# Kernel tuning notes

Measured on AMD Instinct MI355X. Metric: run time of the kernel, lower is better.

Reference implementation:

```python
import jax, jax.numpy as jnp
import numpy as np

B, S, HID = 2, 2048, 1024
NH = 16
HD = HID // NH  # 64
ROPE_BASE = 10000.0
NEG_INF = -1e9


def _rope_emb(seq_len):
    # emb = cat(sin, cos) over head_dim, shape [1, S, 1, HD]
    inv_freq = 1.0 / (ROPE_BASE ** (jnp.arange(0, HD, 2, dtype=jnp.float32) / HD))
    pos = jnp.arange(seq_len, dtype=jnp.float32)
    sincos = pos[:, None] * inv_freq[None, :]            # [S, HD/2]
    emb = jnp.concatenate([jnp.sin(sincos), jnp.cos(sincos)], axis=-1)  # [S, HD]
    return emb[None, :, None, :]


def _apply_rope(x, emb):
    # Faithful to the (quirky) torch code: cos = emb[..., 1::2], sin = emb[..., ::2]
    cos = emb[..., 1::2]
    sin = emb[..., ::2]
    xe = x[..., ::2]
    xo = x[..., 1::2]
    return jnp.concatenate([xe * cos - xo * sin, xe * sin + xo * cos], axis=-1)


def setup_inputs() -> dict:
    key = jax.random.key(0)
    ks = jax.random.split(key, 5)
    hidden_states = jax.random.normal(ks[0], (B, S, HID), dtype=jnp.float32)
    # causal additive mask, broadcast over batch/heads
    causal = jnp.tril(jnp.ones((S, S), dtype=bool))
    attention_mask = jnp.where(causal, 0.0, NEG_INF).astype(jnp.float32)[None, None]
    scale = 1.0 / np.sqrt(HID)
    w_q = jax.random.normal(ks[1], (HID, HID), dtype=jnp.float32) * scale
    w_k = jax.random.normal(ks[2], (HID, HID), dtype=jnp.float32) * scale
    w_v = jax.random.normal(ks[3], (HID, HID), dtype=jnp.float32) * scale
    w_o = jax.random.normal(ks[4], (HID, HID), dtype=jnp.float32) * scale
    return {"hidden_states": hidden_states, "attention_mask": attention_mask,
            "w_q": w_q, "w_k": w_k, "w_v": w_v, "w_o": w_o}


def reference(hidden_states, attention_mask, w_q, w_k, w_v, w_o):
    b, s, _ = hidden_states.shape
    # torch Linear: x @ W.T (W is [out, in])
    q = (hidden_states @ w_q.T).reshape(b, s, NH, HD)
    k = (hidden_states @ w_k.T).reshape(b, s, NH, HD)
    v = (hidden_states @ w_v.T).reshape(b, s, NH, HD)
    emb = _rope_emb(s)
    q = _apply_rope(q, emb)
    k = _apply_rope(k, emb)
    # [b, h, s, d]
    q = q.transpose(0, 2, 1, 3)
    k = k.transpose(0, 2, 1, 3)
    v = v.transpose(0, 2, 1, 3)
    scores = jnp.einsum('bhqd,bhkd->bhqk', q, k) / np.sqrt(HD)
    scores = scores + attention_mask
    attn = jax.nn.softmax(scores, axis=-1)
    out = jnp.einsum('bhqk,bhkd->bhqd', attn, v)
    out = out.transpose(0, 2, 1, 3).reshape(b, s, HID)
    return out @ w_o.T
```

## Files before the change

### kernel.cpp

```cpp
#include <hip/hip_runtime.h>
#include <hip/hip_bf16.h>
#include <math.h>

typedef unsigned short u16;
typedef unsigned int   u32;
typedef unsigned long long u64;
typedef __attribute__((ext_vector_type(8))) short bf16x8;
typedef __attribute__((ext_vector_type(4))) short bf16x4;
typedef __attribute__((ext_vector_type(4))) float f32x4;

#define B_   2
#define S_   2048
#define HID_ 1024
#define NH_  16
#define HD_  64
#define MR_  (B_*S_)

#define QSCALE 0.1803368801111137f
#define MBIAS 32.0f

__device__ __forceinline__ u16 f2bf(float f) {
  union { float f; u32 u; } x; x.f = f;
  u32 r = x.u + 0x7fffu + ((x.u >> 16) & 1u);
  return (u16)(r >> 16);
}
__device__ __forceinline__ void gload16(const void* g, void* l) {
  __builtin_amdgcn_global_load_lds(
      (const __attribute__((address_space(1))) u32*)g,
      (__attribute__((address_space(3))) u32*)l, 16, 0, 0);
}

__global__ void k_cvt_all(const float* __restrict__ hs, const float* __restrict__ wq,
                          const float* __restrict__ wk, const float* __restrict__ wv,
                          const float* __restrict__ wo, ushort4* __restrict__ dst) {
  int i = blockIdx.x * blockDim.x + threadIdx.x;
  const float4* src;
  int idx;
  if (i < 1048576) {
    src = (const float4*)hs; idx = i;
  } else {
    int j = i - 1048576;
    int w = j >> 18; idx = j & 262143;
    src = (const float4*)(w == 0 ? wq : w == 1 ? wk : w == 2 ? wv : wo);
  }
  float4 v = src[idx];
  ushort4 o;
  o.x = f2bf(v.x); o.y = f2bf(v.y); o.z = f2bf(v.z); o.w = f2bf(v.w);
  dst[i] = o;
}

__global__ void k_rope_table(float2* __restrict__ tab) {
  int t = blockIdx.x * blockDim.x + threadIdx.x;
  int p = t >> 5, j = t & 31;
  double fp = (double)p;
  double c, s;
  if (j < 16) {
    s = sin(fp * pow(10000.0, -(2.0 * j) / 32.0));
    c = sin(fp * pow(10000.0, -(2.0 * j + 1.0) / 32.0));
  } else {
    s = cos(fp * pow(10000.0, -(2.0 * j - 32.0) / 32.0));
    c = cos(fp * pow(10000.0, -(2.0 * j - 31.0) / 32.0));
  }
  tab[p * 32 + j] = make_float2((float)c, (float)s);
}

template <int MODE, int BM>
__global__ __launch_bounds__(512) void k_gemm_bt(
    const u16* __restrict__ A,
    const u16* __restrict__ W0, const u16* __restrict__ W1, const u16* __restrict__ W2,
    u16* __restrict__ O0, u16* __restrict__ O1, u16* __restrict__ O2,
    float* __restrict__ OF, const float2* __restrict__ tab, int K) {
  constexpr int WR = BM / 4;
  constexpr int MI = BM / 64;
  __shared__ __align__(16) u16 Al[2][BM * 64];
  __shared__ __align__(16) u16 Bl[2][128 * 64];

  int tid = threadIdx.x;
  int lane = tid & 63, wave = tid >> 6;
  int m0 = blockIdx.y * BM;
  int nt0 = blockIdx.x * 128;
  int wi = nt0 >> 10;
  const u16* W = (wi == 0) ? W0 : (wi == 1 ? W1 : W2);
  int n0 = nt0 & 1023;
  int wm = wave >> 1, wn = wave & 1;
  int lg = lane >> 4, lr = lane & 15;

  f32x4 acc[MI][4];
  const f32x4 vz = {0.f, 0.f, 0.f, 0.f};
#pragma unroll
  for (int i = 0; i < MI; ++i)
#pragma unroll
    for (int j = 0; j < 4; ++j) acc[i][j] = vz;

  auto STAGE = [&](int t_, int bs_) {
    int k0 = t_ * 64;
#pragma unroll
    for (int it = 0; it < BM / 64; ++it) {
      int c = it * 512 + tid;
      int row = c >> 3;
      int cw = (c & 7) ^ (row & 7);
      gload16(&A[(size_t)(m0 + row) * K + k0 + cw * 8], &Al[bs_][(it * 512 + wave * 64) * 8]);
    }
#pragma unroll
    for (int it = 0; it < 2; ++it) {
      int c = it * 512 + tid;
      int row = c >> 3;
      int cw = (c & 7) ^ (row & 7);
      gload16(&W[(size_t)(n0 + row) * K + k0 + cw * 8], &Bl[bs_][(it * 512 + wave * 64) * 8]);
    }
  };

  int nkt = K >> 6;
  STAGE(0, 0);

  for (int t = 0; t < nkt; ++t) {
    int cur = t & 1;
    asm volatile("s_waitcnt vmcnt(0)" ::: "memory");
    __builtin_amdgcn_s_barrier();
    __builtin_amdgcn_sched_barrier(0);
    if (t + 1 < nkt) STAGE(t + 1, cur ^ 1);

#pragma unroll
    for (int kk = 0; kk < 2; ++kk) {
      bf16x8 af[MI], bfr[4];
#pragma unroll
      for (int mi = 0; mi < MI; ++mi) {
        int row = wm * WR + mi * 16 + lr;
        int ci = (kk * 4 + lg) ^ (row & 7);
        af[mi] = *(const bf16x8*)&Al[cur][row * 64 + ci * 8];
      }
#pragma unroll
      for (int ni = 0; ni < 4; ++ni) {
        int row = wn * 64 + ni * 16 + lr;
        int ci = (kk * 4 + lg) ^ (row & 7);
        bfr[ni] = *(const bf16x8*)&Bl[cur][row * 64 + ci * 8];
      }
      __builtin_amdgcn_s_setprio(1);
#pragma unroll
      for (int mi = 0; mi < MI; ++mi)
#pragma unroll
        for (int ni = 0; ni < 4; ++ni)
          acc[mi][ni] = __builtin_amdgcn_mfma_f32_16x16x32_bf16(af[mi], bfr[ni], acc[mi][ni], 0, 0, 0);
      __builtin_amdgcn_s_setprio(0);
    }
  }

  if (MODE == 1) {
#pragma unroll
    for (int mi = 0; mi < MI; ++mi)
#pragma unroll
      for (int ni = 0; ni < 4; ++ni)
#pragma unroll
        for (int r = 0; r < 4; ++r) {
          int grow = m0 + wm * WR + mi * 16 + lg * 4 + r;
          int gcol = n0 + wn * 64 + ni * 16 + lr;
          OF[(size_t)grow * 1024 + gcol] = acc[mi][ni][r];
        }
    return;
  }

  if (wi == 2) {
#pragma unroll
    for (int mi = 0; mi < MI; ++mi) {
      int grow0 = m0 + wm * WR + mi * 16 + lg * 4;
      int bb = grow0 >> 11;
      int s = grow0 & 2047;
#pragma unroll
      for (int ni = 0; ni < 4; ++ni) {
        int gcol = n0 + wn * 64 + ni * 16 + lr;
        int h = gcol >> 6, dd = gcol & 63;
        u64 pk = (u64)f2bf(acc[mi][ni][0]) |
                 ((u64)f2bf(acc[mi][ni][1]) << 16) |
                 ((u64)f2bf(acc[mi][ni][2]) << 32) |
                 ((u64)f2bf(acc[mi][ni][3]) << 48);
        *(u64*)&O2[((size_t)(bb * NH_ + h) * HD_ + dd) * S_ + s] = pk;
      }
    }
  } else {
    u16* OB = wi ? O1 : O0;
    float sc = wi ? 1.0f : QSCALE;
#pragma unroll
    for (int mi = 0; mi < MI; ++mi) {
#pragma unroll
      for (int ni = 0; ni < 4; ++ni) {
        int gcol = n0 + wn * 64 + ni * 16 + lr;
        int h = gcol >> 6;
        int j = (gcol & 63) >> 1;
        bool even = !(gcol & 1);
        int ocol = h * 64 + (even ? j : 32 + j);
#pragma unroll
        for (int r = 0; r < 4; ++r) {
          float val = acc[mi][ni][r];
          float pv = __shfl_xor(val, 1);
          int grow = m0 + wm * WR + mi * 16 + lg * 4 + r;
          int s = grow & 2047;
          float2 cs = tab[s * 32 + j];
          float xe = even ? val : pv;
          float xo = even ? pv : val;
          float res = even ? (xe * cs.x - xo * cs.y) : (xe * cs.y + xo * cs.x);
          OB[(size_t)grow * 1024 + ocol] = f2bf(res * sc);
        }
      }
    }
  }
}

__global__ __launch_bounds__(256, 4) void k_attn(
    const u16* __restrict__ Q, const u16* __restrict__ Kr, const u16* __restrict__ VT,
    u16* __restrict__ O) {
  __shared__ __align__(16) u16 Kl[2][64 * 64];
  __shared__ __align__(16) u16 Vl[2][64 * 64];

  int tid = threadIdx.x, lane = tid & 63, wave = tid >> 6;
  int id = blockIdx.x;
  int qt = 31 - (id >> 5);
  int bh = id & 31;
  int b = bh >> 4, h = bh & 15;
  int lg = lane >> 4, lr = lane & 15;
  int bS = b * S_;
  int nkt = qt + 1;
  int q0 = qt * 64 + wave * 16;

  const u16* vtb = &VT[(size_t)bh * HD_ * S_];
  int l8 = lane >> 3, l7 = lane & 7;
  int sl = l7 ^ l8;

  auto STAGE = [&](int kt_, int bs_) {
#pragma unroll
    for (int it = 0; it < 2; ++it) {
      int rb = wave * 16 + it * 8;
      int r = rb + l8;
      gload16(&Kr[(size_t)(bS + kt_ * 64 + r) * HID_ + h * HD_ + sl * 8],
              &Kl[bs_][rb * 64]);
      gload16(&vtb[(size_t)r * S_ + kt_ * 64 + sl * 8],
              &Vl[bs_][rb * 64]);
    }
  };

  STAGE(0, 0);

  bf16x8 qf[2];
#pragma unroll
  for (int kk = 0; kk < 2; ++kk)
    qf[kk] = *(const bf16x8*)
        &Q[(size_t)(bS + q0 + lr) * HID_ + h * HD_ + kk * 32 + lg * 8];

  f32x4 acc[4];
  const f32x4 vz = {0.f, 0.f, 0.f, 0.f};
#pragma unroll
  for (int df = 0; df < 4; ++df) acc[df] = vz;
  float l_ = 0.f;

  for (int kt = 0; kt < nkt; ++kt) {
    int cur = kt & 1;
    if (kt + 1 < nkt) {
      STAGE(kt + 1, cur ^ 1);
      asm volatile("s_waitcnt vmcnt(4)" ::: "memory");
    } else {
      asm volatile("s_waitcnt vmcnt(0)" ::: "memory");
    }
    __builtin_amdgcn_s_barrier();
    __builtin_amdgcn_sched_barrier(0);

    bf16x8 kfr[4][2];
#pragma unroll
    for (int kf = 0; kf < 4; ++kf) {
      int row = kf * 16 + lr;
#pragma unroll
      for (int kk = 0; kk < 2; ++kk) {
        int ci = (kk * 4 + lg) ^ (row & 7);
        kfr[kf][kk] = *(const bf16x8*)&Kl[cur][row * 64 + ci * 8];
      }
    }

    f32x4 st[4];
#pragma unroll
    for (int kf = 0; kf < 4; ++kf) st[kf] = vz;
    __builtin_amdgcn_s_setprio(1);
#pragma unroll
    for (int kk = 0; kk < 2; ++kk)
#pragma unroll
      for (int kf = 0; kf < 4; ++kf)
        st[kf] = __builtin_amdgcn_mfma_f32_16x16x32_bf16(
            kfr[kf][kk], qf[kk], st[kf], 0, 0, 0);
    __builtin_amdgcn_s_setprio(0);

    if (kt == qt) {
      int qg = q0 + lr;
#pragma unroll
      for (int kf = 0; kf < 4; ++kf)
#pragma unroll
        for (int r = 0; r < 4; ++r) {
          int kg = kt * 64 + kf * 16 + lg * 4 + r;
          if (kg > qg) st[kf][r] = -1e30f;
        }
    }

    float ts = 0.f;
    bf16x4 pb[4];
#pragma unroll
    for (int kf = 0; kf < 4; ++kf) {
#pragma unroll
      for (int r = 0; r < 4; ++r) {
        float e = __builtin_amdgcn_exp2f(st[kf][r] - MBIAS);
        st[kf][r] = e;
        ts += e;
      }
      u32 w0, w1;
      asm("v_cvt_pk_bf16_f32 %0, %1, %2" : "=v"(w0) : "v"(st[kf][0]), "v"(st[kf][1]));
      asm("v_cvt_pk_bf16_f32 %0, %1, %2" : "=v"(w1) : "v"(st[kf][2]), "v"(st[kf][3]));
      union { u32 u[2]; bf16x4 v; } pk;
      pk.u[0] = w0; pk.u[1] = w1;
      pb[kf] = pk.v;
    }
    l_ += ts;

    __builtin_amdgcn_s_setprio(1);
#pragma unroll
    for (int df = 0; df < 4; ++df) {
      int row = df * 16 + lr;
#pragma unroll
      for (int kf = 0; kf < 4; ++kf) {
        int slot = (kf * 2 + (lg >> 1)) ^ (row & 7);
        bf16x4 vfr = *(const bf16x4*)&Vl[cur][row * 64 + slot * 8 + (lg & 1) * 4];
        acc[df] = __builtin_amdgcn_mfma_f32_16x16x16bf16_1k(
            vfr, pb[kf], acc[df], 0, 0, 0);
      }
    }
    __builtin_amdgcn_s_setprio(0);

    __builtin_amdgcn_sched_barrier(0);
    __builtin_amdgcn_s_barrier();
  }

  l_ += __shfl_xor(l_, 16);
  l_ += __shfl_xor(l_, 32);
  float inv = 1.0f / l_;
  int grow = bS + q0 + lr;
#pragma unroll
  for (int df = 0; df < 4; ++df) {
    u64 pk = (u64)f2bf(acc[df][0] * inv) |
             ((u64)f2bf(acc[df][1] * inv) << 16) |
             ((u64)f2bf(acc[df][2] * inv) << 32) |
             ((u64)f2bf(acc[df][3] * inv) << 48);
    *(u64*)&O[(size_t)grow * HID_ + h * HD_ + df * 16 + lg * 4] = pk;
  }
}

extern "C" void kernel_launch(void* const* d_in, const int* in_sizes, int n_in,
                              void* d_out, int out_size, void* d_ws, size_t ws_size,
                              hipStream_t stream) {
  const float* hs = (const float*)d_in[0];
  const float* wq = (const float*)d_in[2];
  const float* wk = (const float*)d_in[3];
  const float* wv = (const float*)d_in[4];
  const float* wo = (const float*)d_in[5];
  float* out = (float*)d_out;

  char* ws = (char*)d_ws;
  const size_t P = (size_t)MR_ * HID_ * 2;
  u16* Xb  = (u16*)(ws);
  u16* Wqb = (u16*)(ws + P);
  u16* Wkb = (u16*)(ws + P + (size_t)HID_ * HID_ * 2);
  u16* Wvb = (u16*)(ws + P + (size_t)HID_ * HID_ * 4);
  u16* Wob = (u16*)(ws + P + (size_t)HID_ * HID_ * 6);
  u16* q_r = (u16*)(ws + 2 * P);
  u16* k_r = (u16*)(ws + 3 * P);
  u16* vt  = (u16*)(ws + 4 * P);
  float2* tab = (float2*)(ws + 5 * P);
  u16* attn_o = Xb;

  k_cvt_all<<<8192, 256, 0, stream>>>(hs, wq, wk, wv, wo, (ushort4*)ws);
  k_rope_table<<<256, 256, 0, stream>>>(tab);

  k_gemm_bt<0, 128><<<dim3(24, 32), 512, 0, stream>>>(
      Xb, Wqb, Wkb, Wvb, q_r, k_r, vt, nullptr, tab, HID_);

  k_attn<<<1024, 256, 0, stream>>>(q_r, k_r, vt, attn_o);

  k_gemm_bt<1, 64><<<dim3(8, 64), 512, 0, stream>>>(
      attn_o, Wob, Wob, Wob, nullptr, nullptr, nullptr, out, nullptr, HID_);
}
```

Before: 115.1 us.

## Use 256x256 tiles with split-K half-stage pipelining for QKV projection

Replaces the templated QKV GEMM (128x128 tiles, 768 blocks) with a dedicated kernel using 256x256 output tiles across 192 blocks. Each 64-wide K step is split into two 32-wide halves with interleaved loads and partial vmcnt waits, so global loads overlap MFMA work. Blocks are assigned to tiles in a grouped order meant to improve L2 reuse. The larger tiles cut redundant global and LDS traffic, but 192 blocks may underfill the CUs and raise register pressure; the O projection is split out unchanged into its own kernel.

After: 119.8 us. +4.1%, slower.

```diff
diff --git a/kernel.cpp b/kernel.cpp
--- a/kernel.cpp
+++ b/kernel.cpp
@@ -64,105 +64,146 @@
   tab[p * 32 + j] = make_float2((float)c, (float)s);
 }
 
-template <int MODE, int BM>
-__global__ __launch_bounds__(512) void k_gemm_bt(
+__global__ __launch_bounds__(512) void k_qkv(
     const u16* __restrict__ A,
     const u16* __restrict__ W0, const u16* __restrict__ W1, const u16* __restrict__ W2,
     u16* __restrict__ O0, u16* __restrict__ O1, u16* __restrict__ O2,
-    float* __restrict__ OF, const float2* __restrict__ tab, int K) {
-  constexpr int WR = BM / 4;
-  constexpr int MI = BM / 64;
-  __shared__ __align__(16) u16 Al[2][BM * 64];
-  __shared__ __align__(16) u16 Bl[2][128 * 64];
+    const float2* __restrict__ tab) {
+  __shared__ __align__(16) u16 Alds[2][2][256 * 32];
+  __shared__ __align__(16) u16 Blds[2][2][256 * 32];
 
   int tid = threadIdx.x;
   int lane = tid & 63, wave = tid >> 6;
-  int m0 = blockIdx.y * BM;
-  int nt0 = blockIdx.x * 128;
-  int wi = nt0 >> 10;
+  int id = blockIdx.x;
+  int g = id >> 3, x = id & 7;
+  int mt = 2 * x + (g & 1);
+  int nt = g >> 1;
+  int m0 = mt * 256;
+  int wi = nt >> 2;
   const u16* W = (wi == 0) ? W0 : (wi == 1 ? W1 : W2);
-  int n0 = nt0 & 1023;
-  int wm = wave >> 1, wn = wave & 1;
+  int n0 = (nt & 3) * 256;
+  int wm = wave >> 2, wn = wave & 3;
   int lg = lane >> 4, lr = lane & 15;
 
-  f32x4 acc[MI][4];
+  f32x4 acc[8][4];
   const f32x4 vz = {0.f, 0.f, 0.f, 0.f};
 #pragma unroll
-  for (int i = 0; i < MI; ++i)
+  for (int i = 0; i < 8; ++i)
 #pragma unroll
     for (int j = 0; j < 4; ++j) acc[i][j] = vz;
 
-  auto STAGE = [&](int t_, int bs_) {
-    int k0 = t_ * 64;
-#pragma unroll
-    for (int it = 0; it < BM / 64; ++it) {
-      int c = it * 512 + tid;
-      int row = c >> 3;
-      int cw = (c & 7) ^ (row & 7);
-      gload16(&A[(size_t)(m0 + row) * K + k0 + cw * 8], &Al[bs_][(it * 512 + wave * 64) * 8]);
-    }
+  auto SA = [&](int j_, int d_, int hk_) {
 #pragma unroll
     for (int it = 0; it < 2; ++it) {
       int c = it * 512 + tid;
-      int row = c >> 3;
-      int cw = (c & 7) ^ (row & 7);
-      gload16(&W[(size_t)(n0 + row) * K + k0 + cw * 8], &Bl[bs_][(it * 512 + wave * 64) * 8]);
+      int row = c >> 2, sl = c & 3;
+      int cw = sl ^ ((row >> 1) & 3);
+      gload16(&A[(size_t)(m0 + row) * HID_ + j_ * 64 + hk_ * 32 + cw * 8],
+              &Alds[d_][hk_][(it * 512 + wave * 64) * 8]);
     }
   };
-
-  int nkt = K >> 6;
-  STAGE(0, 0);
-
-  for (int t = 0; t < nkt; ++t) {
-    int cur = t & 1;
-    asm volatile("s_waitcnt vmcnt(0)" ::: "memory");
+  auto SB = [&](int j_, int d_, int hk_) {
+#pragma unroll
+    for (int it = 0; it < 2; ++it) {
+      int c = it * 512 + tid;
+      int row = c >> 2, sl = c & 3;
+      int cw = sl ^ ((row >> 1) & 3);
+      gload16(&W[(size_t)(n0 + row) * HID_ + j_ * 64 + hk_ * 32 + cw * 8],
+              &Blds[d_][hk_][(it * 512 + wave * 64) * 8]);
+    }
+  };
+
+  SA(0, 0, 0); SB(0, 0, 0); SA(0, 0, 1); SB(0, 0, 1);
+
+  for (int j = 0; j < 16; ++j) {
+    int cur = j & 1, nxt = cur ^ 1;
+    bool more = (j < 15);
+    bf16x8 bfr[4], afr[4];
+
+    asm volatile("s_waitcnt vmcnt(4)" ::: "memory");
     __builtin_amdgcn_s_barrier();
     __builtin_amdgcn_sched_barrier(0);
-    if (t + 1 < nkt) STAGE(t + 1, cur ^ 1);
-
-#pragma unroll
-    for (int kk = 0; kk < 2; ++kk) {
-      bf16x8 af[MI], bfr[4];
-#pragma unroll
-      for (int mi = 0; mi < MI; ++mi) {
-        int row = wm * WR + mi * 16 + lr;
-        int ci = (kk * 4 + lg) ^ (row & 7);
-        af[mi] = *(const bf16x8*)&Al[cur][row * 64 + ci * 8];
-      }
-#pragma unroll
-      for (int ni = 0; ni < 4; ++ni) {
-        int row = wn * 64 + ni * 16 + lr;
-        int ci = (kk * 4 + lg) ^ (row & 7);
-        bfr[ni] = *(const bf16x8*)&Bl[cur][row * 64 + ci * 8];
-      }
-      __builtin_amdgcn_s_setprio(1);
-#pragma unroll
-      for (int mi = 0; mi < MI; ++mi)
-#pragma unroll
-        for (int ni = 0; ni < 4; ++ni)
-          acc[mi][ni] = __builtin_amdgcn_mfma_f32_16x16x32_bf16(af[mi], bfr[ni], acc[mi][ni], 0, 0, 0);
-      __builtin_amdgcn_s_setprio(0);
-    }
-  }
-
-  if (MODE == 1) {
-#pragma unroll
-    for (int mi = 0; mi < MI; ++mi)
+    if (more) SA(j + 1, nxt, 0);
+#pragma unroll
+    for (int ni = 0; ni < 4; ++ni) {
+      int row = wn * 64 + ni * 16 + lr;
+      int ci = lg ^ ((row >> 1) & 3);
+      bfr[ni] = *(const bf16x8*)&Blds[cur][0][row * 32 + ci * 8];
+    }
+#pragma unroll
+    for (int mi = 0; mi < 4; ++mi) {
+      int row = wm * 128 + mi * 16 + lr;
+      int ci = lg ^ ((row >> 1) & 3);
+      afr[mi] = *(const bf16x8*)&Alds[cur][0][row * 32 + ci * 8];
+    }
+    __builtin_amdgcn_s_setprio(1);
+#pragma unroll
+    for (int mi = 0; mi < 4; ++mi)
 #pragma unroll
       for (int ni = 0; ni < 4; ++ni)
-#pragma unroll
-        for (int r = 0; r < 4; ++r) {
-          int grow = m0 + wm * WR + mi * 16 + lg * 4 + r;
-          int gcol = n0 + wn * 64 + ni * 16 + lr;
-          OF[(size_t)grow * 1024 + gcol] = acc[mi][ni][r];
-        }
-    return;
+        acc[mi][ni] = __builtin_amdgcn_mfma_f32_16x16x32_bf16(afr[mi], bfr[ni], acc[mi][ni], 0, 0, 0);
+    __builtin_amdgcn_s_setprio(0);
+
+    if (more) SB(j + 1, nxt, 0);
+#pragma unroll
+    for (int mi = 0; mi < 4; ++mi) {
+      int row = wm * 128 + (mi + 4) * 16 + lr;
+      int ci = lg ^ ((row >> 1) & 3);
+      afr[mi] = *(const bf16x8*)&Alds[cur][0][row * 32 + ci * 8];
+    }
+    __builtin_amdgcn_s_setprio(1);
+#pragma unroll
+    for (int mi = 0; mi < 4; ++mi)
+#pragma unroll
+      for (int ni = 0; ni < 4; ++ni)
+        acc[mi + 4][ni] = __builtin_amdgcn_mfma_f32_16x16x32_bf16(afr[mi], bfr[ni], acc[mi + 4][ni], 0, 0, 0);
+    __builtin_amdgcn_s_setprio(0);
+
+    if (more) { asm volatile("s_waitcnt vmcnt(4)" ::: "memory"); }
+    else      { asm volatile("s_waitcnt vmcnt(0)" ::: "memory"); }
+    __builtin_amdgcn_s_barrier();
+    __builtin_amdgcn_sched_barrier(0);
+    if (more) SA(j + 1, nxt, 1);
+#pragma unroll
+    for (int ni = 0; ni < 4; ++ni) {
+      int row = wn * 64 + ni * 16 + lr;
+      int ci = lg ^ ((row >> 1) & 3);
+      bfr[ni] = *(const bf16x8*)&Blds[cur][1][row * 32 + ci * 8];
+    }
+#pragma unroll
+    for (int mi = 0; mi < 4; ++mi) {
+      int row = wm * 128 + mi * 16 + lr;
+      int ci = lg ^ ((row >> 1) & 3);
+      afr[mi] = *(const bf16x8*)&Alds[cur][1][row * 32 + ci * 8];
+    }
+    __builtin_amdgcn_s_setprio(1);
+#pragma unroll
+    for (int mi = 0; mi < 4; ++mi)
+#pragma unroll
+      for (int ni = 0; ni < 4; ++ni)
+        acc[mi][ni] = __builtin_amdgcn_mfma_f32_16x16x32_bf16(afr[mi], bfr[ni], acc[mi][ni], 0, 0, 0);
+    __builtin_amdgcn_s_setprio(0);
+
+    if (more) SB(j + 1, nxt, 1);
+#pragma unroll
+    for (int mi = 0; mi < 4; ++mi) {
+      int row = wm * 128 + (mi + 4) * 16 + lr;
+      int ci = lg ^ ((row >> 1) & 3);
+      afr[mi] = *(const bf16x8*)&Alds[cur][1][row * 32 + ci * 8];
+    }
+    __builtin_amdgcn_s_setprio(1);
+#pragma unroll
+    for (int mi = 0; mi < 4; ++mi)
+#pragma unroll
+      for (int ni = 0; ni < 4; ++ni)
+        acc[mi + 4][ni] = __builtin_amdgcn_mfma_f32_16x16x32_bf16(afr[mi], bfr[ni], acc[mi + 4][ni], 0, 0, 0);
+    __builtin_amdgcn_s_setprio(0);
   }
 
   if (wi == 2) {
 #pragma unroll
-    for (int mi = 0; mi < MI; ++mi) {
-      int grow0 = m0 + wm * WR + mi * 16 + lg * 4;
+    for (int mi = 0; mi < 8; ++mi) {
+      int grow0 = m0 + wm * 128 + mi * 16 + lg * 4;
       int bb = grow0 >> 11;
       int s = grow0 & 2047;
 #pragma unroll
@@ -180,7 +221,7 @@
     u16* OB = wi ? O1 : O0;
     float sc = wi ? 1.0f : QSCALE;
 #pragma unroll
-    for (int mi = 0; mi < MI; ++mi) {
+    for (int mi = 0; mi < 8; ++mi) {
 #pragma unroll
       for (int ni = 0; ni < 4; ++ni) {
         int gcol = n0 + wn * 64 + ni * 16 + lr;
@@ -192,7 +233,7 @@
         for (int r = 0; r < 4; ++r) {
           float val = acc[mi][ni][r];
           float pv = __shfl_xor(val, 1);
-          int grow = m0 + wm * WR + mi * 16 + lg * 4 + r;
+          int grow = m0 + wm * 128 + mi * 16 + lg * 4 + r;
           int s = grow & 2047;
           float2 cs = tab[s * 32 + j];
           float xe = even ? val : pv;
@@ -203,6 +244,83 @@
       }
     }
   }
+}
+
+__global__ __launch_bounds__(512) void k_oproj(
+    const u16* __restrict__ A, const u16* __restrict__ W0,
+    float* __restrict__ OF, int K) {
+  __shared__ __align__(16) u16 Al[2][64 * 64];
+  __shared__ __align__(16) u16 Bl[2][128 * 64];
+
+  int tid = threadIdx.x;
+  int lane = tid & 63, wave = tid >> 6;
+  int m0 = blockIdx.y * 64;
+  int n0 = blockIdx.x * 128;
+  int wm = wave >> 1, wn = wave & 1;
+  int lg = lane >> 4, lr = lane & 15;
+
+  f32x4 acc[4];
+  const f32x4 vz = {0.f, 0.f, 0.f, 0.f};
+#pragma unroll
+  for (int j = 0; j < 4; ++j) acc[j] = vz;
+
+  auto STAGE = [&](int t_, int bs_) {
+    int k0 = t_ * 64;
+    {
+      int c = tid;
+      int row = c >> 3;
+      int cw = (c & 7) ^ (row & 7);
+      gload16(&A[(size_t)(m0 + row) * K + k0 + cw * 8], &Al[bs_][(wave * 64) * 8]);
+    }
+#pragma unroll
+    for (int it = 0; it < 2; ++it) {
+      int c = it * 512 + tid;
+      int row = c >> 3;
+      int cw = (c & 7) ^ (row & 7);
+      gload16(&W0[(size_t)(n0 + row) * K + k0 + cw * 8], &Bl[bs_][(it * 512 + wave * 64) * 8]);
+    }
+  };
+
+  int nkt = K >> 6;
+  STAGE(0, 0);
+
+  for (int t = 0; t < nkt; ++t) {
+    int cur = t & 1;
+    asm volatile("s_waitcnt vmcnt(0)" ::: "memory");
+    __builtin_amdgcn_s_barrier();
+    __builtin_amdgcn_sched_barrier(0);
+    if (t + 1 < nkt) STAGE(t + 1, cur ^ 1);
+
+#pragma unroll
+    for (int kk = 0; kk < 2; ++kk) {
+      bf16x8 af, bfr[4];
+      {
+        int row = wm * 16 + lr;
+        int ci = (kk * 4 + lg) ^ (row & 7);
+        af = *(const bf16x8*)&Al[cur][row * 64 + ci * 8];
+      }
+#pragma unroll
+      for (int ni = 0; ni < 4; ++ni) {
+        int row = wn * 64 + ni * 16 + lr;
+        int ci = (kk * 4 + lg) ^ (row & 7);
+        bfr[ni] = *(const bf16x8*)&Bl[cur][row * 64 + ci * 8];
+      }
+      __builtin_amdgcn_s_setprio(1);
+#pragma unroll
+      for (int ni = 0; ni < 4; ++ni)
+        acc[ni] = __builtin_amdgcn_mfma_f32_16x16x32_bf16(af, bfr[ni], acc[ni], 0, 0, 0);
+      __builtin_amdgcn_s_setprio(0);
+    }
+  }
+
+#pragma unroll
+  for (int ni = 0; ni < 4; ++ni)
+#pragma unroll
+    for (int r = 0; r < 4; ++r) {
+      int grow = m0 + wm * 16 + lg * 4 + r;
+      int gcol = n0 + wn * 64 + ni * 16 + lr;
+      OF[(size_t)grow * 1024 + gcol] = acc[ni][r];
+    }
 }
 
 __global__ __launch_bounds__(256, 4) void k_attn(
@@ -373,11 +491,9 @@
   k_cvt_all<<<8192, 256, 0, stream>>>(hs, wq, wk, wv, wo, (ushort4*)ws);
   k_rope_table<<<256, 256, 0, stream>>>(tab);
 
-  k_gemm_bt<0, 128><<<dim3(24, 32), 512, 0, stream>>>(
-      Xb, Wqb, Wkb, Wvb, q_r, k_r, vt, nullptr, tab, HID_);
+  k_qkv<<<192, 512, 0, stream>>>(Xb, Wqb, Wkb, Wvb, q_r, k_r, vt, tab);
 
   k_attn<<<1024, 256, 0, stream>>>(q_r, k_r, vt, attn_o);
 
-  k_gemm_bt<1, 64><<<dim3(8, 64), 512, 0, stream>>>(
-      attn_o, Wob, Wob, Wob, nullptr, nullptr, nullptr, out, nullptr, HID_);
-}
+  k_oproj<<<dim3(8, 64), 512, 0, stream>>>(attn_o, Wob, out, HID_);
+}
```
